# Performance work log

Measured on AMD Instinct MI355X. Metric: run time of the kernel, lower is better.

The kernel has to match this reference:

```python
import jax, jax.numpy as jnp
import numpy as np


def setup_inputs() -> dict:
    key = jax.random.key(0)
    qkv = jax.random.normal(key, (2, 1536, 4096), dtype=jnp.float32)
    return {"qkv": qkv, "num_heads": 8}


def reference(qkv, num_heads):
    bs, width, length = qkv.shape
    ch = width // (3 * num_heads)
    # [B*H, 3*ch, T] -> split into q, k, v each [B*H, ch, T]
    qkv_h = qkv.reshape(bs * num_heads, 3 * ch, length)
    q, k, v = qkv_h[:, :ch], qkv_h[:, ch:2 * ch], qkv_h[:, 2 * ch:]
    scale = 1.0 / np.sqrt(np.sqrt(ch)).astype(np.float32)
    # scores: [B*H, T, T]
    weight = jnp.einsum('bct,bcs->bts', q * scale, k * scale)
    weight = jax.nn.softmax(weight.astype(jnp.float32), axis=-1).astype(weight.dtype)
    a = jnp.einsum('bts,bcs->bct', weight, v)  # [B*H, ch, T]
    return a.reshape(bs, num_heads * ch, length)
```

## Files before the change

kernel.cpp:

```cpp
#include <hip/hip_runtime.h>
#include <hip/hip_bf16.h>

typedef __bf16 bf16x8 __attribute__((ext_vector_type(8)));
typedef __bf16 bf16x4 __attribute__((ext_vector_type(4)));
typedef __bf16 bf16x2 __attribute__((ext_vector_type(2)));
typedef float  f32x4  __attribute__((ext_vector_type(4)));

#define T_LEN 4096
#define QBLK  128
#define KVBLK 64
#define NKV   (T_LEN / KVBLK)

__device__ __forceinline__ int swz(int row, int colByte) {
    return row * 128 + (colByte ^ (((row ^ (row >> 2)) & 7) << 4));
}
__device__ __forceinline__ int swzM(int row, int colByte) {
    return row * 128 + (colByte ^ ((row & 7) << 4));
}
__device__ __forceinline__ int swzO(int row, int colByte) {
    return row * 512 + (colByte ^ ((row & 7) << 5));
}

#define QSCALE 0.18033688011112042f

#if __has_builtin(__builtin_amdgcn_exp2f)
#define EXP2(x) __builtin_amdgcn_exp2f(x)
#else
__device__ __forceinline__ float EXP2(float x) {
    float r; asm("v_exp_f32 %0, %1" : "=v"(r) : "v"(x)); return r;
}
#endif

__device__ __forceinline__ void glds16(const void* g, void* l) {
    __builtin_amdgcn_global_load_lds(
        (const __attribute__((address_space(1))) void*)g,
        (__attribute__((address_space(3))) void*)l, 16, 0, 0);
}

__global__ __launch_bounds__(256)
void qkv_prepass(const float* __restrict__ qkv, char* __restrict__ kpan,
                 char* __restrict__ vpan) {
    const int tile = blockIdx.x;
    const int bh   = blockIdx.y;
    const float* kp = qkv + ((size_t)bh * 192 + 64)  * T_LEN + tile * 64;
    const float* vp = qkv + ((size_t)bh * 192 + 128) * T_LEN + tile * 64;
    char* kout = kpan + (size_t)(bh * 64 + tile) * 8192;
    char* vout = vpan + (size_t)(bh * 64 + tile) * 8192;

    const int t  = threadIdx.x;
    const int s  = t & 63;
    const int o4 = t >> 6;
    #pragma unroll
    for (int oo = 0; oo < 2; ++oo) {
        const int oct = o4 + oo * 4;
        bf16x8 v;
        #pragma unroll
        for (int j = 0; j < 8; ++j)
            v[j] = (__bf16)kp[(size_t)(oct * 8 + j) * T_LEN + s];
        *(bf16x8*)(kout + swz(s, oct * 16)) = v;
    }
    const int c = t & 63;
    #pragma unroll
    for (int p = 0; p < 4; ++p) {
        const int u = o4 * 4 + p;
        float4 f = *(const float4*)(vp + (size_t)c * T_LEN + u * 4);
        const int up = (u & 8) | ((u & 3) << 1) | ((u >> 2) & 1);
        bf16x4 hv;
        hv[0] = (__bf16)f.x; hv[1] = (__bf16)f.y;
        hv[2] = (__bf16)f.z; hv[3] = (__bf16)f.w;
        *(bf16x4*)(vout + swz(c, up * 8)) = hv;
    }
}

__global__ __launch_bounds__(512, 4)
void qkv_attn_glds(const float* __restrict__ qkv, float* __restrict__ out,
                   const char* __restrict__ kpan, const char* __restrict__ vpan) {
    __shared__ __align__(16) char lds[49664];

    const int fid   = (blockIdx.x & 7) * 64 + (blockIdx.x >> 3);
    const int bh    = fid >> 5;
    const int ttile = fid & 31;
    const float* qp = qkv + (size_t)bh * 192 * T_LEN;
    const char* kpb = kpan + (size_t)bh * 64 * 8192;
    const char* vpb = vpan + (size_t)bh * 64 * 8192;
    const int t0 = ttile * QBLK;

    const int tid  = threadIdx.x;
    const int wave = tid >> 6, lane = tid & 63;
    const int g = lane >> 4, i = lane & 15;
    const int tg = wave >> 1, half = wave & 1;

    glds16(kpb + tid * 16, lds + 16384 + wave * 1024);
    glds16(vpb + tid * 16, lds + 32768 + wave * 1024);

    {
        const int tq  = (tid & 31) * 4;
        const int cp8 = tid >> 5;
        #pragma unroll
        for (int hh = 0; hh < 2; ++hh) {
            const int cpair = cp8 + hh * 16;
            const float* base = qp + (size_t)(cpair * 2) * T_LEN + t0 + tq;
            float4 lo = *(const float4*)(base);
            float4 hi = *(const float4*)(base + T_LEN);
            bf16x2 v;
            v[0] = (__bf16)(lo.x * QSCALE); v[1] = (__bf16)(hi.x * QSCALE);
            *(bf16x2*)(lds + swz(tq + 0, cpair * 4)) = v;
            v[0] = (__bf16)(lo.y * QSCALE); v[1] = (__bf16)(hi.y * QSCALE);
            *(bf16x2*)(lds + swz(tq + 1, cpair * 4)) = v;
            v[0] = (__bf16)(lo.z * QSCALE); v[1] = (__bf16)(hi.z * QSCALE);
            *(bf16x2*)(lds + swz(tq + 2, cpair * 4)) = v;
            v[0] = (__bf16)(lo.w * QSCALE); v[1] = (__bf16)(hi.w * QSCALE);
            *(bf16x2*)(lds + swz(tq + 3, cpair * 4)) = v;
        }
    }
    __syncthreads();
    bf16x8 qreg[2][2];
    #pragma unroll
    for (int h = 0; h < 2; ++h)
        #pragma unroll
        for (int kk = 0; kk < 2; ++kk)
            qreg[h][kk] = *(const bf16x8*)(lds + swz(tg * 32 + h * 16 + i, kk * 64 + g * 16));

    f32x4 oacc[2][4];
    #pragma unroll
    for (int h = 0; h < 2; ++h)
        #pragma unroll
        for (int n = 0; n < 4; ++n) oacc[h][n] = (f32x4){0.f, 0.f, 0.f, 0.f};
    float l0 = 0.f, l1 = 0.f;

    for (int kv = 0; kv < NKV; ++kv) {
        if (kv + 1 < NKV) {
            const int b = (kv + 1) & 1;
            glds16(kpb + (size_t)(kv + 1) * 8192 + tid * 16,
                   lds + 16384 + b * 8192 + wave * 1024);
            glds16(vpb + (size_t)(kv + 1) * 8192 + tid * 16,
                   lds + 32768 + b * 8192 + wave * 1024);
        }
        char* KsR = lds + 16384 + (kv & 1) * 8192;
        char* VsR = lds + 32768 + (kv & 1) * 8192;
        f32x4 sacc[2][2];
        #pragma unroll
        for (int h = 0; h < 2; ++h)
            #pragma unroll
            for (int mt = 0; mt < 2; ++mt) sacc[h][mt] = (f32x4){0.f, 0.f, 0.f, 0.f};
        #pragma unroll
        for (int kk = 0; kk < 2; ++kk)
            #pragma unroll
            for (int mt = 0; mt < 2; ++mt) {
                bf16x8 kf = *(const bf16x8*)(KsR + swz(half * 32 + mt * 16 + i, kk * 64 + g * 16));
                sacc[0][mt] = __builtin_amdgcn_mfma_f32_16x16x32_bf16(kf, qreg[0][kk], sacc[0][mt], 0, 0, 0);
                sacc[1][mt] = __builtin_amdgcn_mfma_f32_16x16x32_bf16(kf, qreg[1][kk], sacc[1][mt], 0, 0, 0);
            }
        float rs0 = 0.f, rs1 = 0.f;
        bf16x8 pa0, pa1;
        #pragma unroll
        for (int r = 0; r < 4; ++r) {
            float a0 = EXP2(sacc[0][0][r]);
            float a1 = EXP2(sacc[0][1][r]);
            rs0 += a0 + a1;
            pa0[r] = (__bf16)a0; pa0[4 + r] = (__bf16)a1;
            float b0 = EXP2(sacc[1][0][r]);
            float b1 = EXP2(sacc[1][1][r]);
            rs1 += b0 + b1;
            pa1[r] = (__bf16)b0; pa1[4 + r] = (__bf16)b1;
        }
        #pragma unroll
        for (int n = 0; n < 4; ++n) {
            bf16x8 bv = *(const bf16x8*)(VsR + swz(n * 16 + i, half * 64 + g * 16));
            oacc[0][n] = __builtin_amdgcn_mfma_f32_16x16x32_bf16(pa0, bv, oacc[0][n], 0, 0, 0);
            oacc[1][n] = __builtin_amdgcn_mfma_f32_16x16x32_bf16(pa1, bv, oacc[1][n], 0, 0, 0);
        }
        rs0 += __shfl_xor(rs0, 16); rs0 += __shfl_xor(rs0, 32);
        rs1 += __shfl_xor(rs1, 16); rs1 += __shfl_xor(rs1, 32);
        l0 += rs0; l1 += rs1;
        __syncthreads();
    }

    char* mbase = lds + 16384 + tg * 8192;
    float* lbase = (float*)(lds + 49152);
    if (half == 1) {
        #pragma unroll
        for (int h = 0; h < 2; ++h)
            #pragma unroll
            for (int n = 0; n < 4; ++n)
                *(f32x4*)(mbase + swzM(n * 16 + i, h * 64 + g * 16)) = oacc[h][n];
        if (g == 0) { lbase[tg * 32 + i] = l0; lbase[tg * 32 + 16 + i] = l1; }
    }
    __syncthreads();
    if (half == 0) {
        #pragma unroll
        for (int h = 0; h < 2; ++h)
            #pragma unroll
            for (int n = 0; n < 4; ++n)
                oacc[h][n] += *(const f32x4*)(mbase + swzM(n * 16 + i, h * 64 + g * 16));
        l0 += lbase[tg * 32 + i];
        l1 += lbase[tg * 32 + 16 + i];
    }
    __syncthreads();
    if (half == 0) {
        #pragma unroll
        for (int h = 0; h < 2; ++h) {
            float invl = 1.0f / (h ? l1 : l0);
            #pragma unroll
            for (int reg = 0; reg < 4; ++reg) {
                float inv_r = __shfl(invl, g * 4 + reg);
                int t_loc = tg * 32 + h * 16 + g * 4 + reg;
                #pragma unroll
                for (int n = 0; n < 4; ++n) {
                    int c = n * 16 + i;
                    *(float*)(lds + swzO(c, t_loc * 4)) = oacc[h][n][reg] * inv_r;
                }
            }
        }
    }
    __syncthreads();
    #pragma unroll
    for (int it = 0; it < 4; ++it) {
        int idx = it * 512 + tid;
        int c   = idx >> 5;
        int seg = idx & 31;
        float4 u = *(const float4*)(lds + swzO(c, seg * 16));
        *(float4*)(out + (size_t)(bh * 64 + c) * T_LEN + t0 + seg * 4) = u;
    }
}

__global__ __launch_bounds__(512, 4)
void qkv_attn_fb(const float* __restrict__ qkv, float* __restrict__ out) {
    __shared__ __align__(16) char lds[66560];
    const int fid   = (blockIdx.x & 7) * 64 + (blockIdx.x >> 3);
    const int bh    = fid >> 5;
    const int ttile = fid & 31;
    const float* qp = qkv + (size_t)bh * 192 * T_LEN;
    const float* kp = qp + (size_t)64  * T_LEN;
    const float* vp = qp + (size_t)128 * T_LEN;
    const int t0 = ttile * QBLK;
    const int tid  = threadIdx.x;
    const int wave = tid >> 6, lane = tid & 63;
    const int g = lane >> 4, i = lane & 15;
    const int tg = wave >> 1, half = wave & 1;
    const int k_c  = tid >> 4;
    const int k_sq = (tid & 15) * 4;
    const float* kbase = kp + (size_t)(k_c * 2) * T_LEN + k_sq;
    const int v_c  = tid >> 3;
    const int v_u0 = (tid & 7) * 2;
    const float* vbase = vp + (size_t)v_c * T_LEN + v_u0 * 4;
    {
        const int tq  = (tid & 31) * 4;
        const int cp8 = tid >> 5;
        #pragma unroll
        for (int hh = 0; hh < 2; ++hh) {
            const int cpair = cp8 + hh * 16;
            const float* base = qp + (size_t)(cpair * 2) * T_LEN + t0 + tq;
            float4 lo = *(const float4*)(base);
            float4 hi = *(const float4*)(base + T_LEN);
            bf16x2 v;
            v[0] = (__bf16)(lo.x * QSCALE); v[1] = (__bf16)(hi.x * QSCALE);
            *(bf16x2*)(lds + swz(tq + 0, cpair * 4)) = v;
            v[0] = (__bf16)(lo.y * QSCALE); v[1] = (__bf16)(hi.y * QSCALE);
            *(bf16x2*)(lds + swz(tq + 1, cpair * 4)) = v;
            v[0] = (__bf16)(lo.z * QSCALE); v[1] = (__bf16)(hi.z * QSCALE);
            *(bf16x2*)(lds + swz(tq + 2, cpair * 4)) = v;
            v[0] = (__bf16)(lo.w * QSCALE); v[1] = (__bf16)(hi.w * QSCALE);
            *(bf16x2*)(lds + swz(tq + 3, cpair * 4)) = v;
        }
    }
    {
        float4 lo = *(const float4*)(kbase);
        float4 hi = *(const float4*)(kbase + T_LEN);
        bf16x2 w;
        char* KsW = lds + 16384;
        w[0] = (__bf16)lo.x; w[1] = (__bf16)hi.x; *(bf16x2*)(KsW + swz(k_sq + 0, k_c * 4)) = w;
        w[0] = (__bf16)lo.y; w[1] = (__bf16)hi.y; *(bf16x2*)(KsW + swz(k_sq + 1, k_c * 4)) = w;
        w[0] = (__bf16)lo.z; w[1] = (__bf16)hi.z; *(bf16x2*)(KsW + swz(k_sq + 2, k_c * 4)) = w;
        w[0] = (__bf16)lo.w; w[1] = (__bf16)hi.w; *(bf16x2*)(KsW + swz(k_sq + 3, k_c * 4)) = w;
        char* VsW = lds + 32768;
        #pragma unroll
        for (int p = 0; p < 2; ++p) {
            int u  = v_u0 + p;
            int up = (u & 8) | ((u & 3) << 1) | ((u >> 2) & 1);
            float4 f = *(const float4*)(vbase + p * 4);
            bf16x4 hv;
            hv[0] = (__bf16)f.x; hv[1] = (__bf16)f.y;
            hv[2] = (__bf16)f.z; hv[3] = (__bf16)f.w;
            *(bf16x4*)(VsW + swz(v_c, up * 8)) = hv;
        }
    }
    __syncthreads();
    bf16x8 qreg[2][2];
    #pragma unroll
    for (int h = 0; h < 2; ++h)
        #pragma unroll
        for (int kk = 0; kk < 2; ++kk)
            qreg[h][kk] = *(const bf16x8*)(lds + swz(tg * 32 + h * 16 + i, kk * 64 + g * 16));
    f32x4 oacc[2][4];
    #pragma unroll
    for (int h = 0; h < 2; ++h)
        #pragma unroll
        for (int n = 0; n < 4; ++n) oacc[h][n] = (f32x4){0.f, 0.f, 0.f, 0.f};
    float l0 = 0.f, l1 = 0.f;
    for (int kv = 0; kv < NKV; ++kv) {
        const int s0n = (kv + 1 < NKV) ? (kv + 1) * KVBLK : 0;
        float4 klo = *(const float4*)(kbase + s0n);
        float4 khi = *(const float4*)(kbase + T_LEN + s0n);
        float4 vl0 = *(const float4*)(vbase + s0n);
        float4 vl1 = *(const float4*)(vbase + s0n + 4);
        char* KsR = lds + 16384 + (kv & 1) * 8192;
        char* VsR = lds + 32768 + (kv & 1) * 8192;
        f32x4 sacc[2][2];
        #pragma unroll
        for (int h = 0; h < 2; ++h)
            #pragma unroll
            for (int mt = 0; mt < 2; ++mt) sacc[h][mt] = (f32x4){0.f, 0.f, 0.f, 0.f};
        #pragma unroll
        for (int kk = 0; kk < 2; ++kk)
            #pragma unroll
            for (int mt = 0; mt < 2; ++mt) {
                bf16x8 kf = *(const bf16x8*)(KsR + swz(half * 32 + mt * 16 + i, kk * 64 + g * 16));
                sacc[0][mt] = __builtin_amdgcn_mfma_f32_16x16x32_bf16(kf, qreg[0][kk], sacc[0][mt], 0, 0, 0);
                sacc[1][mt] = __builtin_amdgcn_mfma_f32_16x16x32_bf16(kf, qreg[1][kk], sacc[1][mt], 0, 0, 0);
            }
        float rs0 = 0.f, rs1 = 0.f;
        bf16x8 pa0, pa1;
        #pragma unroll
        for (int r = 0; r < 4; ++r) {
            float a0 = EXP2(sacc[0][0][r]);
            float a1 = EXP2(sacc[0][1][r]);
            rs0 += a0 + a1;
            pa0[r] = (__bf16)a0; pa0[4 + r] = (__bf16)a1;
            float b0 = EXP2(sacc[1][0][r]);
            float b1 = EXP2(sacc[1][1][r]);
            rs1 += b0 + b1;
            pa1[r] = (__bf16)b0; pa1[4 + r] = (__bf16)b1;
        }
        #pragma unroll
        for (int n = 0; n < 4; ++n) {
            bf16x8 bv = *(const bf16x8*)(VsR + swz(n * 16 + i, half * 64 + g * 16));
            oacc[0][n] = __builtin_amdgcn_mfma_f32_16x16x32_bf16(pa0, bv, oacc[0][n], 0, 0, 0);
            oacc[1][n] = __builtin_amdgcn_mfma_f32_16x16x32_bf16(pa1, bv, oacc[1][n], 0, 0, 0);
        }
        rs0 += __shfl_xor(rs0, 16); rs0 += __shfl_xor(rs0, 32);
        rs1 += __shfl_xor(rs1, 16); rs1 += __shfl_xor(rs1, 32);
        l0 += rs0; l1 += rs1;
        if (kv + 1 < NKV) {
            char* KsW = lds + 16384 + ((kv + 1) & 1) * 8192;
            char* VsW = lds + 32768 + ((kv + 1) & 1) * 8192;
            bf16x2 w;
            w[0] = (__bf16)klo.x; w[1] = (__bf16)khi.x; *(bf16x2*)(KsW + swz(k_sq + 0, k_c * 4)) = w;
            w[0] = (__bf16)klo.y; w[1] = (__bf16)khi.y; *(bf16x2*)(KsW + swz(k_sq + 1, k_c * 4)) = w;
            w[0] = (__bf16)klo.z; w[1] = (__bf16)khi.z; *(bf16x2*)(KsW + swz(k_sq + 2, k_c * 4)) = w;
            w[0] = (__bf16)klo.w; w[1] = (__bf16)khi.w; *(bf16x2*)(KsW + swz(k_sq + 3, k_c * 4)) = w;
            #pragma unroll
            for (int p = 0; p < 2; ++p) {
                int u  = v_u0 + p;
                int up = (u & 8) | ((u & 3) << 1) | ((u >> 2) & 1);
                float4 f = p ? vl1 : vl0;
                bf16x4 hv;
                hv[0] = (__bf16)f.x; hv[1] = (__bf16)f.y;
                hv[2] = (__bf16)f.z; hv[3] = (__bf16)f.w;
                *(bf16x4*)(VsW + swz(v_c, up * 8)) = hv;
            }
        }
        __syncthreads();
    }
    char* mbase = lds + 32768 + tg * 8192;
    float* lbase = (float*)(lds + 65536);
    if (half == 1) {
        #pragma unroll
        for (int h = 0; h < 2; ++h)
            #pragma unroll
            for (int n = 0; n < 4; ++n)
                *(f32x4*)(mbase + swzM(n * 16 + i, h * 64 + g * 16)) = oacc[h][n];
        if (g == 0) { lbase[tg * 32 + i] = l0; lbase[tg * 32 + 16 + i] = l1; }
    }
    __syncthreads();
    if (half == 0) {
        #pragma unroll
        for (int h = 0; h < 2; ++h)
            #pragma unroll
            for (int n = 0; n < 4; ++n)
                oacc[h][n] += *(const f32x4*)(mbase + swzM(n * 16 + i, h * 64 + g * 16));
        l0 += lbase[tg * 32 + i];
        l1 += lbase[tg * 32 + 16 + i];
        #pragma unroll
        for (int h = 0; h < 2; ++h) {
            float invl = 1.0f / (h ? l1 : l0);
            #pragma unroll
            for (int reg = 0; reg < 4; ++reg) {
                float inv_r = __shfl(invl, g * 4 + reg);
                int t_loc = tg * 32 + h * 16 + g * 4 + reg;
                #pragma unroll
                for (int n = 0; n < 4; ++n) {
                    int c = n * 16 + i;
                    *(float*)(lds + swzO(c, t_loc * 4)) = oacc[h][n][reg] * inv_r;
                }
            }
        }
    }
    __syncthreads();
    #pragma unroll
    for (int it = 0; it < 4; ++it) {
        int idx = it * 512 + tid;
        int c   = idx >> 5;
        int seg = idx & 31;
        float4 u = *(const float4*)(lds + swzO(c, seg * 16));
        *(float4*)(out + (size_t)(bh * 64 + c) * T_LEN + t0 + seg * 4) = u;
    }
}

extern "C" void kernel_launch(void* const* d_in, const int* in_sizes, int n_in,
                              void* d_out, int out_size, void* d_ws, size_t ws_size,
                              hipStream_t stream) {
    const float* qkv = (const float*)d_in[0];
    float* out = (float*)d_out;
    const size_t pan_bytes = (size_t)16 * 64 * 8192;
    if (ws_size >= 2 * pan_bytes) {
        char* kpan = (char*)d_ws;
        char* vpan = kpan + pan_bytes;
        qkv_prepass<<<dim3(64, 16), 256, 0, stream>>>(qkv, kpan, vpan);
        qkv_attn_glds<<<dim3(512), 512, 0, stream>>>(qkv, out, kpan, vpan);
    } else {
        qkv_attn_fb<<<dim3(512), 512, 0, stream>>>(qkv, out);
    }
}
```

Measured before the change: 96.57 us.

## Process two KV tiles per barrier and defer row-sum shuffles to loop end

The main attention kernel now loads two 64-column K/V tiles per iteration into larger double-buffered LDS, halving the number of __syncthreads barriers and async-load phases. Row-sum cross-lane shuffles are moved out of the KV loop in both kernels, so each lane accumulates partial sums and reduces once at the end. The cost is LDS growing from about 49 KB to 80 KB per block, which may lower occupancy against the launch bound of 4 blocks per CU.

```diff
diff --git a/kernel.cpp b/kernel.cpp
--- a/kernel.cpp
+++ b/kernel.cpp
@@ -8,8 +8,8 @@
 
 #define T_LEN 4096
 #define QBLK  128
-#define KVBLK 64
-#define NKV   (T_LEN / KVBLK)
+#define NKV   64
+#define NIT   32
 
 __device__ __forceinline__ int swz(int row, int colByte) {
     return row * 128 + (colByte ^ (((row ^ (row >> 2)) & 7) << 4));
@@ -75,7 +75,7 @@
 __global__ __launch_bounds__(512, 4)
 void qkv_attn_glds(const float* __restrict__ qkv, float* __restrict__ out,
                    const char* __restrict__ kpan, const char* __restrict__ vpan) {
-    __shared__ __align__(16) char lds[49664];
+    __shared__ __align__(16) char lds[81920];
 
     const int fid   = (blockIdx.x & 7) * 64 + (blockIdx.x >> 3);
     const int bh    = fid >> 5;
@@ -90,8 +90,10 @@
     const int g = lane >> 4, i = lane & 15;
     const int tg = wave >> 1, half = wave & 1;
 
-    glds16(kpb + tid * 16, lds + 16384 + wave * 1024);
-    glds16(vpb + tid * 16, lds + 32768 + wave * 1024);
+    glds16(kpb + tid * 16,        lds + 16384 + wave * 1024);
+    glds16(kpb + 8192 + tid * 16, lds + 16384 + 8192 + wave * 1024);
+    glds16(vpb + tid * 16,        lds + 49152 + wave * 1024);
+    glds16(vpb + 8192 + tid * 16, lds + 49152 + 8192 + wave * 1024);
 
     {
         const int tq  = (tid & 31) * 4;
@@ -128,56 +130,58 @@
         for (int n = 0; n < 4; ++n) oacc[h][n] = (f32x4){0.f, 0.f, 0.f, 0.f};
     float l0 = 0.f, l1 = 0.f;
 
-    for (int kv = 0; kv < NKV; ++kv) {
-        if (kv + 1 < NKV) {
-            const int b = (kv + 1) & 1;
-            glds16(kpb + (size_t)(kv + 1) * 8192 + tid * 16,
-                   lds + 16384 + b * 8192 + wave * 1024);
-            glds16(vpb + (size_t)(kv + 1) * 8192 + tid * 16,
-                   lds + 32768 + b * 8192 + wave * 1024);
-        }
-        char* KsR = lds + 16384 + (kv & 1) * 8192;
-        char* VsR = lds + 32768 + (kv & 1) * 8192;
-        f32x4 sacc[2][2];
-        #pragma unroll
-        for (int h = 0; h < 2; ++h)
-            #pragma unroll
-            for (int mt = 0; mt < 2; ++mt) sacc[h][mt] = (f32x4){0.f, 0.f, 0.f, 0.f};
-        #pragma unroll
-        for (int kk = 0; kk < 2; ++kk)
-            #pragma unroll
-            for (int mt = 0; mt < 2; ++mt) {
-                bf16x8 kf = *(const bf16x8*)(KsR + swz(half * 32 + mt * 16 + i, kk * 64 + g * 16));
-                sacc[0][mt] = __builtin_amdgcn_mfma_f32_16x16x32_bf16(kf, qreg[0][kk], sacc[0][mt], 0, 0, 0);
-                sacc[1][mt] = __builtin_amdgcn_mfma_f32_16x16x32_bf16(kf, qreg[1][kk], sacc[1][mt], 0, 0, 0);
-            }
-        float rs0 = 0.f, rs1 = 0.f;
-        bf16x8 pa0, pa1;
-        #pragma unroll
-        for (int r = 0; r < 4; ++r) {
-            float a0 = EXP2(sacc[0][0][r]);
-            float a1 = EXP2(sacc[0][1][r]);
-            rs0 += a0 + a1;
-            pa0[r] = (__bf16)a0; pa0[4 + r] = (__bf16)a1;
-            float b0 = EXP2(sacc[1][0][r]);
-            float b1 = EXP2(sacc[1][1][r]);
-            rs1 += b0 + b1;
-            pa1[r] = (__bf16)b0; pa1[4 + r] = (__bf16)b1;
-        }
-        #pragma unroll
-        for (int n = 0; n < 4; ++n) {
-            bf16x8 bv = *(const bf16x8*)(VsR + swz(n * 16 + i, half * 64 + g * 16));
-            oacc[0][n] = __builtin_amdgcn_mfma_f32_16x16x32_bf16(pa0, bv, oacc[0][n], 0, 0, 0);
-            oacc[1][n] = __builtin_amdgcn_mfma_f32_16x16x32_bf16(pa1, bv, oacc[1][n], 0, 0, 0);
-        }
-        rs0 += __shfl_xor(rs0, 16); rs0 += __shfl_xor(rs0, 32);
-        rs1 += __shfl_xor(rs1, 16); rs1 += __shfl_xor(rs1, 32);
-        l0 += rs0; l1 += rs1;
+    for (int it = 0; it < NIT; ++it) {
+        if (it + 1 < NIT) {
+            const size_t off = (size_t)(2 * it + 2) * 8192;
+            const int b = (it + 1) & 1;
+            glds16(kpb + off + tid * 16,        lds + 16384 + b * 16384 + wave * 1024);
+            glds16(kpb + off + 8192 + tid * 16, lds + 16384 + b * 16384 + 8192 + wave * 1024);
+            glds16(vpb + off + tid * 16,        lds + 49152 + b * 16384 + wave * 1024);
+            glds16(vpb + off + 8192 + tid * 16, lds + 49152 + b * 16384 + 8192 + wave * 1024);
+        }
+        #pragma unroll
+        for (int ta = 0; ta < 2; ++ta) {
+            char* KsR = lds + 16384 + (it & 1) * 16384 + ta * 8192;
+            char* VsR = lds + 49152 + (it & 1) * 16384 + ta * 8192;
+            f32x4 sacc[2][2];
+            #pragma unroll
+            for (int h = 0; h < 2; ++h)
+                #pragma unroll
+                for (int mt = 0; mt < 2; ++mt) sacc[h][mt] = (f32x4){0.f, 0.f, 0.f, 0.f};
+            #pragma unroll
+            for (int kk = 0; kk < 2; ++kk)
+                #pragma unroll
+                for (int mt = 0; mt < 2; ++mt) {
+                    bf16x8 kf = *(const bf16x8*)(KsR + swz(half * 32 + mt * 16 + i, kk * 64 + g * 16));
+                    sacc[0][mt] = __builtin_amdgcn_mfma_f32_16x16x32_bf16(kf, qreg[0][kk], sacc[0][mt], 0, 0, 0);
+                    sacc[1][mt] = __builtin_amdgcn_mfma_f32_16x16x32_bf16(kf, qreg[1][kk], sacc[1][mt], 0, 0, 0);
+                }
+            bf16x8 pa0, pa1;
+            #pragma unroll
+            for (int r = 0; r < 4; ++r) {
+                float a0 = EXP2(sacc[0][0][r]);
+                float a1 = EXP2(sacc[0][1][r]);
+                l0 += a0 + a1;
+                pa0[r] = (__bf16)a0; pa0[4 + r] = (__bf16)a1;
+                float b0 = EXP2(sacc[1][0][r]);
+                float b1 = EXP2(sacc[1][1][r]);
+                l1 += b0 + b1;
+                pa1[r] = (__bf16)b0; pa1[4 + r] = (__bf16)b1;
+            }
+            #pragma unroll
+            for (int n = 0; n < 4; ++n) {
+                bf16x8 bv = *(const bf16x8*)(VsR + swz(n * 16 + i, half * 64 + g * 16));
+                oacc[0][n] = __builtin_amdgcn_mfma_f32_16x16x32_bf16(pa0, bv, oacc[0][n], 0, 0, 0);
+                oacc[1][n] = __builtin_amdgcn_mfma_f32_16x16x32_bf16(pa1, bv, oacc[1][n], 0, 0, 0);
+            }
+        }
         __syncthreads();
     }
+    l0 += __shfl_xor(l0, 16); l0 += __shfl_xor(l0, 32);
+    l1 += __shfl_xor(l1, 16); l1 += __shfl_xor(l1, 32);
 
     char* mbase = lds + 16384 + tg * 8192;
-    float* lbase = (float*)(lds + 49152);
+    float* lbase = (float*)(lds);
     if (half == 1) {
         #pragma unroll
         for (int h = 0; h < 2; ++h)
@@ -298,8 +302,8 @@
         #pragma unroll
         for (int n = 0; n < 4; ++n) oacc[h][n] = (f32x4){0.f, 0.f, 0.f, 0.f};
     float l0 = 0.f, l1 = 0.f;
-    for (int kv = 0; kv < NKV; ++kv) {
-        const int s0n = (kv + 1 < NKV) ? (kv + 1) * KVBLK : 0;
+    for (int kv = 0; kv < 64; ++kv) {
+        const int s0n = (kv + 1 < 64) ? (kv + 1) * 64 : 0;
         float4 klo = *(const float4*)(kbase + s0n);
         float4 khi = *(const float4*)(kbase + T_LEN + s0n);
         float4 vl0 = *(const float4*)(vbase + s0n);
@@ -319,17 +323,16 @@
                 sacc[0][mt] = __builtin_amdgcn_mfma_f32_16x16x32_bf16(kf, qreg[0][kk], sacc[0][mt], 0, 0, 0);
                 sacc[1][mt] = __builtin_amdgcn_mfma_f32_16x16x32_bf16(kf, qreg[1][kk], sacc[1][mt], 0, 0, 0);
             }
-        float rs0 = 0.f, rs1 = 0.f;
         bf16x8 pa0, pa1;
         #pragma unroll
         for (int r = 0; r < 4; ++r) {
             float a0 = EXP2(sacc[0][0][r]);
             float a1 = EXP2(sacc[0][1][r]);
-            rs0 += a0 + a1;
+            l0 += a0 + a1;
             pa0[r] = (__bf16)a0; pa0[4 + r] = (__bf16)a1;
             float b0 = EXP2(sacc[1][0][r]);
             float b1 = EXP2(sacc[1][1][r]);
-            rs1 += b0 + b1;
+            l1 += b0 + b1;
             pa1[r] = (__bf16)b0; pa1[4 + r] = (__bf16)b1;
         }
         #pragma unroll
@@ -338,10 +341,7 @@
             oacc[0][n] = __builtin_amdgcn_mfma_f32_16x16x32_bf16(pa0, bv, oacc[0][n], 0, 0, 0);
             oacc[1][n] = __builtin_amdgcn_mfma_f32_16x16x32_bf16(pa1, bv, oacc[1][n], 0, 0, 0);
         }
-        rs0 += __shfl_xor(rs0, 16); rs0 += __shfl_xor(rs0, 32);
-        rs1 += __shfl_xor(rs1, 16); rs1 += __shfl_xor(rs1, 32);
-        l0 += rs0; l1 += rs1;
-        if (kv + 1 < NKV) {
+        if (kv + 1 < 64) {
             char* KsW = lds + 16384 + ((kv + 1) & 1) * 8192;
             char* VsW = lds + 32768 + ((kv + 1) & 1) * 8192;
             bf16x2 w;
@@ -362,6 +362,8 @@
         }
         __syncthreads();
     }
+    l0 += __shfl_xor(l0, 16); l0 += __shfl_xor(l0, 32);
+    l1 += __shfl_xor(l1, 16); l1 += __shfl_xor(l1, 32);
     char* mbase = lds + 32768 + tg * 8192;
     float* lbase = (float*)(lds + 65536);
     if (half == 1) {
```

After: 92.09 us. -4.6%, faster.
